# Optimization experiments

Hardware: AMD Instinct MI355X
Metric: run time of the kernel (lower is better)

The kernel has to match this reference:

```python
import jax, jax.numpy as jnp
import numpy as np

B, S, D = 2, 2048, 1024
H = 16
DH = D // H  # 64


def setup_inputs() -> dict:
    key = jax.random.key(0)
    k1, k2, k3 = jax.random.split(key, 3)
    X = jax.random.normal(k1, (B, S, D), dtype=jnp.float32)
    # xavier_normal for Linear(D, 3*D): std = sqrt(2/(fan_in+fan_out))
    std_qkv = float(np.sqrt(2.0 / (D + 3 * D)))
    std_out = float(np.sqrt(2.0 / (D + D)))
    W_qkv = jax.random.normal(k2, (3 * H * DH, D), dtype=jnp.float32) * std_qkv
    W_out = jax.random.normal(k3, (D, H * DH), dtype=jnp.float32) * std_out
    return {"X": X, "W_qkv": W_qkv, "W_out": W_out}


def reference(X, W_qkv, W_out):
    b, s, d = X.shape
    # stacked projection: (b, s, 3*H*DH), then per-head chunk into q,k,v
    qkv = jnp.einsum('bsd,ed->bse', X, W_qkv)
    qkv = qkv.reshape(b, s, H, 3 * DH)
    q, k, v = jnp.split(qkv, 3, axis=-1)  # each (b, s, H, DH)
    scale = 1.0 / jnp.sqrt(jnp.asarray(DH, dtype=X.dtype))
    # naive unfused attention: full [b,H,s,s] score matrix
    scores = jnp.einsum('bqhd,bkhd->bhqk', q, k) * scale
    attn = jax.nn.softmax(scores, axis=-1)
    vals = jnp.einsum('bhqk,bkhd->bqhd', attn, v)
    vals = vals.reshape(b, s, H * DH)
    out = jnp.einsum('bse,de->bsd', vals, W_out)
    return out
```

## Files before the change

### kernel.cpp

```cpp
#include <hip/hip_runtime.h>
#include <cstdint>
#include <cstddef>

typedef __bf16 bf16;
typedef __bf16 bf16x8 __attribute__((ext_vector_type(8)));
typedef __bf16 bf16x2 __attribute__((ext_vector_type(2)));
typedef float  floatx4 __attribute__((ext_vector_type(4)));

typedef __attribute__((address_space(1))) void gvoid_t;
typedef __attribute__((address_space(3))) void lvoid_t;

#define MFMA16(a, b, c) __builtin_amdgcn_mfma_f32_16x16x32_bf16((a), (b), (c), 0, 0, 0)

#if __has_builtin(__builtin_amdgcn_exp2f)
#define EXP2(x) __builtin_amdgcn_exp2f(x)
#else
#define EXP2(x) exp2f(x)
#endif

#define S_TOK 2048
#define E3 3072
#define DMODEL 1024

#define NX 4194304
#define NWQ 3145728
#define NWO 1048576
__global__ __launch_bounds__(256) void cvt_all(const float* __restrict__ X,
                                               const float* __restrict__ Wq,
                                               const float* __restrict__ Wo,
                                               bf16* __restrict__ Xb,
                                               bf16* __restrict__ Wqb,
                                               bf16* __restrict__ Wob) {
  int i = (blockIdx.x * 256 + threadIdx.x) * 8;
  const float* s;
  bf16* d;
  float sc = 1.0f;
  int off;
  if (i < NX) {
    s = X; d = Xb; off = i;
  } else if (i < NX + NWQ) {
    off = i - NX; s = Wq; d = Wqb;
    int row = off >> 10;
    if ((row % 192) < 64) sc = 0.18033688011f;
  } else {
    off = i - NX - NWQ; s = Wo; d = Wob;
  }
  const float4* p = (const float4*)(s + off);
  float4 a = p[0], b = p[1];
  bf16x8 o;
  o[0] = (bf16)(a.x * sc); o[1] = (bf16)(a.y * sc);
  o[2] = (bf16)(a.z * sc); o[3] = (bf16)(a.w * sc);
  o[4] = (bf16)(b.x * sc); o[5] = (bf16)(b.y * sc);
  o[6] = (bf16)(b.z * sc); o[7] = (bf16)(b.w * sc);
  *(bf16x8*)(d + off) = o;
}

__device__ __forceinline__ void gl_lds16(const bf16* g, bf16* l) {
  __builtin_amdgcn_global_load_lds((gvoid_t*)g, (lvoid_t*)l, 16, 0, 0);
}

template <bool OUT_BF16, bool FUSE_V>
__global__ __launch_bounds__(256) void gemm_bt(const bf16* __restrict__ A,
                                               const bf16* __restrict__ Bt,
                                               void* __restrict__ Cv,
                                               bf16* __restrict__ Vt,
                                               int M, int N, int K) {
  __shared__ bf16 sA[128 * 64];
  __shared__ bf16 sB[128 * 64];
  const int tid = threadIdx.x;
  const int wv = tid >> 6, lane = tid & 63;
  const int wr = wv >> 1, wc = wv & 1;
  const int lrow = lane & 15, lgrp = lane >> 4;
  const int R0 = blockIdx.y * 128, C0 = blockIdx.x * 128;

  floatx4 acc[4][4] = {};

  const int srow = lane >> 3;
  const int schk = (lane & 7) ^ srow;
  const bf16* gA = A + (size_t)(R0 + wv * 32 + srow) * K + schk * 8;
  const bf16* gB = Bt + (size_t)(C0 + wv * 32 + srow) * K + schk * 8;
  bf16* lA = sA + wv * 32 * 64;
  bf16* lB = sB + wv * 32 * 64;
  const size_t rs8 = (size_t)8 * K;

  for (int k0 = 0; k0 < K; k0 += 64) {
#pragma unroll
    for (int c = 0; c < 4; c++) {
      gl_lds16(gA + k0 + c * rs8, lA + c * 512);
      gl_lds16(gB + k0 + c * rs8, lB + c * 512);
    }
    __syncthreads();
#pragma unroll
    for (int kk = 0; kk < 2; kk++) {
      bf16x8 af[4], bfr[4];
#pragma unroll
      for (int i = 0; i < 4; i++) {
        int r = wr * 64 + i * 16 + lrow;
        af[i] = *(const bf16x8*)&sA[r * 64 + ((kk * 4 + lgrp) ^ (r & 7)) * 8];
      }
#pragma unroll
      for (int j = 0; j < 4; j++) {
        int r = wc * 64 + j * 16 + lrow;
        bfr[j] = *(const bf16x8*)&sB[r * 64 + ((kk * 4 + lgrp) ^ (r & 7)) * 8];
      }
#pragma unroll
      for (int i = 0; i < 4; i++)
#pragma unroll
        for (int j = 0; j < 4; j++)
          acc[i][j] = MFMA16(af[i], bfr[j], acc[i][j]);
    }
    __syncthreads();
  }

  const int rbase = R0 + wr * 64 + lgrp * 4;
  const int cbase = C0 + wc * 64 + lrow;
  if (OUT_BF16) {
    bf16* C = (bf16*)Cv;
#pragma unroll
    for (int i = 0; i < 4; i++)
#pragma unroll
      for (int j = 0; j < 4; j++) {
        const int col = cbase + j * 16;
        const int m192 = col % 192;
        const int hh = col / 192;
#pragma unroll
        for (int r = 0; r < 4; r++) {
          const int row = rbase + i * 16 + r;
          bf16 val = (bf16)acc[i][j][r];
          bf16* dst;
          if (FUSE_V && m192 >= 128) {
            const int sl = row & 2047;
            const int sp = (sl & ~31) | ((sl & 15) << 1) | ((sl >> 4) & 1);
            dst = Vt + ((size_t)(((row >> 11) * 16 + hh) * 64 + (m192 - 128))) * S_TOK + sp;
          } else {
            dst = C + (size_t)row * N + col;
          }
          *dst = val;
        }
      }
  } else {
    float* C = (float*)Cv;
#pragma unroll
    for (int i = 0; i < 4; i++)
#pragma unroll
      for (int j = 0; j < 4; j++)
#pragma unroll
        for (int r = 0; r < 4; r++)
          C[(size_t)(rbase + i * 16 + r) * N + cbase + j * 16] = acc[i][j][r];
  }
}

__global__ __launch_bounds__(256) void gemm_bt_n64(const bf16* __restrict__ A,
                                                   const bf16* __restrict__ Bt,
                                                   float* __restrict__ C,
                                                   int M, int N, int K) {
  __shared__ bf16 sA[128 * 64];
  __shared__ bf16 sB[64 * 64];
  const int tid = threadIdx.x;
  const int wv = tid >> 6, lane = tid & 63;
  const int wr = wv >> 1, wc = wv & 1;
  const int lrow = lane & 15, lgrp = lane >> 4;
  const int R0 = blockIdx.y * 128, C0 = blockIdx.x * 64;

  floatx4 acc[4][2] = {};

  const int srow = lane >> 3;
  const int schk = (lane & 7) ^ srow;
  const bf16* gA = A + (size_t)(R0 + wv * 32 + srow) * K + schk * 8;
  const bf16* gB = Bt + (size_t)(C0 + wv * 16 + srow) * K + schk * 8;
  bf16* lA = sA + wv * 32 * 64;
  bf16* lB = sB + wv * 16 * 64;
  const size_t rs8 = (size_t)8 * K;

  for (int k0 = 0; k0 < K; k0 += 64) {
#pragma unroll
    for (int c = 0; c < 4; c++) gl_lds16(gA + k0 + c * rs8, lA + c * 512);
#pragma unroll
    for (int c = 0; c < 2; c++) gl_lds16(gB + k0 + c * rs8, lB + c * 512);
    __syncthreads();
#pragma unroll
    for (int kk = 0; kk < 2; kk++) {
      bf16x8 af[4], bfr[2];
#pragma unroll
      for (int i = 0; i < 4; i++) {
        int r = wr * 64 + i * 16 + lrow;
        af[i] = *(const bf16x8*)&sA[r * 64 + ((kk * 4 + lgrp) ^ (r & 7)) * 8];
      }
#pragma unroll
      for (int j = 0; j < 2; j++) {
        int r = wc * 32 + j * 16 + lrow;
        bfr[j] = *(const bf16x8*)&sB[r * 64 + ((kk * 4 + lgrp) ^ (r & 7)) * 8];
      }
#pragma unroll
      for (int i = 0; i < 4; i++)
#pragma unroll
        for (int j = 0; j < 2; j++)
          acc[i][j] = MFMA16(af[i], bfr[j], acc[i][j]);
    }
    __syncthreads();
  }

  const int rbase = R0 + wr * 64 + lgrp * 4;
  const int cbase = C0 + wc * 32 + lrow;
#pragma unroll
  for (int i = 0; i < 4; i++)
#pragma unroll
    for (int j = 0; j < 2; j++)
#pragma unroll
      for (int r = 0; r < 4; r++)
        C[(size_t)(rbase + i * 16 + r) * N + cbase + j * 16] = acc[i][j][r];
}

__global__ __launch_bounds__(512, 2) void attn(const bf16* __restrict__ qkv,
                                               const bf16* __restrict__ Vt,
                                               bf16* __restrict__ vals) {
  __shared__ bf16 sK[2][128 * 64];
  __shared__ bf16 sV[2][64 * 128];
  __shared__ bf16 sP[8][2][640];

  const int tid = threadIdx.x;
  const int wv = tid >> 6, lane = tid & 63;
  const int lrow = lane & 15, lgrp = lane >> 4;
  const int b = blockIdx.z, h = blockIdx.y;
  const int qb = blockIdx.x * 256;

  const int srow = lane >> 3;
  const int scol = (lane & 7) ^ srow;
  const bf16* kg0 = qkv + (size_t)(b * S_TOK + wv * 8 + srow) * E3 + h * 192 + 64 + scol * 8;
  const int vrow = lane >> 4;
  const int vchk = lane & 15;
  const int d0 = wv * 8 + vrow, d1 = d0 + 4;
  const bf16* vg0 = Vt + (size_t)((b * 16 + h) * 64 + d0) * S_TOK + (vchk ^ (d0 & 15)) * 8;
  const bf16* vg1 = Vt + (size_t)((b * 16 + h) * 64 + d1) * S_TOK + (vchk ^ (d1 & 15)) * 8;

  const bf16* qp = qkv + (size_t)(b * S_TOK + qb + wv * 32) * E3 + h * 192;
  bf16x8 qa[2][2];
#pragma unroll
  for (int rt = 0; rt < 2; rt++)
#pragma unroll
    for (int dh = 0; dh < 2; dh++)
      qa[rt][dh] = *(const bf16x8*)(qp + (size_t)(rt * 16 + lrow) * E3 + dh * 32 + lgrp * 8);

  floatx4 O[2][4] = {};
  floatx4 lacc[2] = {};
  bf16x8 ones;
  const bf16 one1 = (bf16)1.0f;
#pragma unroll
  for (int j = 0; j < 8; j++) ones[j] = one1;

  auto stage = [&](int buf, int st) {
    const bf16* kg = kg0 + (size_t)st * 128 * E3;
    gl_lds16(kg, &sK[buf][wv * 512]);
    gl_lds16(kg + (size_t)64 * E3, &sK[buf][4096 + wv * 512]);
    gl_lds16(vg0 + st * 128, &sV[buf][wv * 1024]);
    gl_lds16(vg1 + st * 128, &sV[buf][wv * 1024 + 512]);
  };

  auto compute = [&](int buf) {
#pragma unroll
    for (int g = 0; g < 4; g++) {
      bf16x8 kf[2][2];
#pragma unroll
      for (int t = 0; t < 2; t++)
#pragma unroll
        for (int dh = 0; dh < 2; dh++)
          kf[t][dh] = *(const bf16x8*)&sK[buf][(g * 32 + t * 16 + lrow) * 64 +
                                              ((dh * 4 + lgrp) ^ (lrow & 7)) * 8];
#pragma unroll
      for (int rt = 0; rt < 2; rt++) {
        floatx4 sc0 = {0.f, 0.f, 0.f, 0.f}, sc1 = {0.f, 0.f, 0.f, 0.f};
        sc0 = MFMA16(qa[rt][0], kf[0][0], sc0);
        sc0 = MFMA16(qa[rt][1], kf[0][1], sc0);
        sc1 = MFMA16(qa[rt][0], kf[1][0], sc1);
        sc1 = MFMA16(qa[rt][1], kf[1][1], sc1);
#pragma unroll
        for (int r = 0; r < 4; r++) {
          bf16x2 h2;
          h2[0] = (bf16)EXP2(sc0[r]);
          h2[1] = (bf16)EXP2(sc1[r]);
          *(unsigned*)&sP[wv][rt][(lgrp * 4 + r) * 40 + lrow * 2] =
              __builtin_bit_cast(unsigned, h2);
        }
      }
      bf16x8 vf[4];
#pragma unroll
      for (int dt = 0; dt < 4; dt++)
        vf[dt] = *(const bf16x8*)&sV[buf][(dt * 16 + lrow) * 128 +
                                          ((g * 4 + lgrp) ^ lrow) * 8];
#pragma unroll
      for (int rt = 0; rt < 2; rt++) {
        bf16x8 pf = *(const bf16x8*)&sP[wv][rt][lrow * 40 + lgrp * 8];
#pragma unroll
        for (int dt = 0; dt < 4; dt++) O[rt][dt] = MFMA16(pf, vf[dt], O[rt][dt]);
        lacc[rt] = MFMA16(pf, ones, lacc[rt]);
      }
    }
  };

  stage(0, 0);
  __syncthreads();
#pragma unroll 1
  for (int st = 0; st < 16; st += 2) {
    stage(1, st + 1);
    compute(0);
    __syncthreads();
    if (st + 2 < 16) stage(0, st + 2);
    compute(1);
    __syncthreads();
  }

  bf16* vout = vals + (size_t)(b * S_TOK + qb + wv * 32) * DMODEL + h * 64;
#pragma unroll
  for (int rt = 0; rt < 2; rt++)
#pragma unroll
    for (int r = 0; r < 4; r++) {
      float rinv = __builtin_amdgcn_rcpf(lacc[rt][r]);
#pragma unroll
      for (int dt = 0; dt < 4; dt++)
        vout[(size_t)(rt * 16 + lgrp * 4 + r) * DMODEL + dt * 16 + lrow] =
            (bf16)(O[rt][dt][r] * rinv);
    }
}

extern "C" void kernel_launch(void* const* d_in, const int* in_sizes, int n_in,
                              void* d_out, int out_size, void* d_ws, size_t ws_size,
                              hipStream_t stream) {
  const float* X = (const float*)d_in[0];
  const float* Wqkv = (const float*)d_in[1];
  const float* Wout = (const float*)d_in[2];
  float* out = (float*)d_out;

  char* ws = (char*)d_ws;
  bf16* Xb = (bf16*)(ws);
  bf16* Wqb = (bf16*)(ws + ((size_t)8 << 20));
  bf16* Wob = (bf16*)(ws + ((size_t)14 << 20));
  bf16* qkvb = (bf16*)(ws + ((size_t)16 << 20));
  bf16* Vt = (bf16*)(ws + ((size_t)40 << 20));
  bf16* vals = (bf16*)(ws + ((size_t)48 << 20));

  cvt_all<<<(NX + NWQ + NWO) / 2048, 256, 0, stream>>>(X, Wqkv, Wout, Xb, Wqb, Wob);

  gemm_bt<true, true><<<dim3(24, 32), 256, 0, stream>>>(Xb, Wqb, qkvb, Vt, 4096, 3072, 1024);

  attn<<<dim3(8, 16, 2), 512, 0, stream>>>(qkvb, Vt, vals);

  gemm_bt_n64<<<dim3(16, 32), 256, 0, stream>>>(vals, Wob, out, 4096, 1024, 1024);
}
```

Before: 178.0 us.

## Software-pipeline QK/exp/PV stages in attention with double-buffered P tiles

Splits the per-group attention body into QK, exp-and-write-P, and PV stages, then interleaves them so the exp work of one group overlaps the MFMAs of another. The P scratch tile is double-buffered to allow this. MFMA sections are wrapped in s_setprio raises to favor matrix issue across waves. The grid is also reordered so heads vary fastest, which changes block scheduling and L2 locality; the extra P buffer raises LDS use.

```diff
diff --git a/kernel.cpp b/kernel.cpp
--- a/kernel.cpp
+++ b/kernel.cpp
@@ -216,13 +216,13 @@
                                                bf16* __restrict__ vals) {
   __shared__ bf16 sK[2][128 * 64];
   __shared__ bf16 sV[2][64 * 128];
-  __shared__ bf16 sP[8][2][640];
+  __shared__ bf16 sP[8][2][2][640];
 
   const int tid = threadIdx.x;
   const int wv = tid >> 6, lane = tid & 63;
   const int lrow = lane & 15, lgrp = lane >> 4;
-  const int b = blockIdx.z, h = blockIdx.y;
-  const int qb = blockIdx.x * 256;
+  const int b = blockIdx.z, h = blockIdx.x;
+  const int qb = blockIdx.y * 256;
 
   const int srow = lane >> 3;
   const int scol = (lane & 7) ^ srow;
@@ -243,6 +243,7 @@
 
   floatx4 O[2][4] = {};
   floatx4 lacc[2] = {};
+  floatx4 sc[2][2];
   bf16x8 ones;
   const bf16 one1 = (bf16)1.0f;
 #pragma unroll
@@ -256,45 +257,66 @@
     gl_lds16(vg1 + st * 128, &sV[buf][wv * 1024 + 512]);
   };
 
+  auto qk_g = [&](int buf, int g) {
+    bf16x8 kf[2][2];
+#pragma unroll
+    for (int t = 0; t < 2; t++)
+#pragma unroll
+      for (int dh = 0; dh < 2; dh++)
+        kf[t][dh] = *(const bf16x8*)&sK[buf][(g * 32 + t * 16 + lrow) * 64 +
+                                            ((dh * 4 + lgrp) ^ (lrow & 7)) * 8];
+    __builtin_amdgcn_s_setprio(1);
+#pragma unroll
+    for (int rt = 0; rt < 2; rt++) {
+      floatx4 a0 = {0.f, 0.f, 0.f, 0.f}, a1 = {0.f, 0.f, 0.f, 0.f};
+      a0 = MFMA16(qa[rt][0], kf[0][0], a0);
+      a0 = MFMA16(qa[rt][1], kf[0][1], a0);
+      a1 = MFMA16(qa[rt][0], kf[1][0], a1);
+      a1 = MFMA16(qa[rt][1], kf[1][1], a1);
+      sc[rt][0] = a0;
+      sc[rt][1] = a1;
+    }
+    __builtin_amdgcn_s_setprio(0);
+  };
+
+  auto expw_g = [&](int g) {
+#pragma unroll
+    for (int rt = 0; rt < 2; rt++)
+#pragma unroll
+      for (int r = 0; r < 4; r++) {
+        bf16x2 h2;
+        h2[0] = (bf16)EXP2(sc[rt][0][r]);
+        h2[1] = (bf16)EXP2(sc[rt][1][r]);
+        *(unsigned*)&sP[wv][rt][g & 1][(lgrp * 4 + r) * 40 + lrow * 2] =
+            __builtin_bit_cast(unsigned, h2);
+      }
+  };
+
+  auto pv_g = [&](int buf, int g) {
+    bf16x8 vf[4];
+#pragma unroll
+    for (int dt = 0; dt < 4; dt++)
+      vf[dt] = *(const bf16x8*)&sV[buf][(dt * 16 + lrow) * 128 + ((g * 4 + lgrp) ^ lrow) * 8];
+    __builtin_amdgcn_s_setprio(1);
+#pragma unroll
+    for (int rt = 0; rt < 2; rt++) {
+      bf16x8 pf = *(const bf16x8*)&sP[wv][rt][g & 1][lrow * 40 + lgrp * 8];
+#pragma unroll
+      for (int dt = 0; dt < 4; dt++) O[rt][dt] = MFMA16(pf, vf[dt], O[rt][dt]);
+      lacc[rt] = MFMA16(pf, ones, lacc[rt]);
+    }
+    __builtin_amdgcn_s_setprio(0);
+  };
+
   auto compute = [&](int buf) {
-#pragma unroll
-    for (int g = 0; g < 4; g++) {
-      bf16x8 kf[2][2];
-#pragma unroll
-      for (int t = 0; t < 2; t++)
-#pragma unroll
-        for (int dh = 0; dh < 2; dh++)
-          kf[t][dh] = *(const bf16x8*)&sK[buf][(g * 32 + t * 16 + lrow) * 64 +
-                                              ((dh * 4 + lgrp) ^ (lrow & 7)) * 8];
-#pragma unroll
-      for (int rt = 0; rt < 2; rt++) {
-        floatx4 sc0 = {0.f, 0.f, 0.f, 0.f}, sc1 = {0.f, 0.f, 0.f, 0.f};
-        sc0 = MFMA16(qa[rt][0], kf[0][0], sc0);
-        sc0 = MFMA16(qa[rt][1], kf[0][1], sc0);
-        sc1 = MFMA16(qa[rt][0], kf[1][0], sc1);
-        sc1 = MFMA16(qa[rt][1], kf[1][1], sc1);
-#pragma unroll
-        for (int r = 0; r < 4; r++) {
-          bf16x2 h2;
-          h2[0] = (bf16)EXP2(sc0[r]);
-          h2[1] = (bf16)EXP2(sc1[r]);
-          *(unsigned*)&sP[wv][rt][(lgrp * 4 + r) * 40 + lrow * 2] =
-              __builtin_bit_cast(unsigned, h2);
-        }
-      }
-      bf16x8 vf[4];
-#pragma unroll
-      for (int dt = 0; dt < 4; dt++)
-        vf[dt] = *(const bf16x8*)&sV[buf][(dt * 16 + lrow) * 128 +
-                                          ((g * 4 + lgrp) ^ lrow) * 8];
-#pragma unroll
-      for (int rt = 0; rt < 2; rt++) {
-        bf16x8 pf = *(const bf16x8*)&sP[wv][rt][lrow * 40 + lgrp * 8];
-#pragma unroll
-        for (int dt = 0; dt < 4; dt++) O[rt][dt] = MFMA16(pf, vf[dt], O[rt][dt]);
-        lacc[rt] = MFMA16(pf, ones, lacc[rt]);
-      }
-    }
+    qk_g(buf, 0); expw_g(0);
+    qk_g(buf, 1); expw_g(1);
+    pv_g(buf, 0);
+    qk_g(buf, 2); expw_g(2);
+    pv_g(buf, 1);
+    qk_g(buf, 3); expw_g(3);
+    pv_g(buf, 2);
+    pv_g(buf, 3);
   };
 
   stage(0, 0);
@@ -342,7 +364,7 @@
 
   gemm_bt<true, true><<<dim3(24, 32), 256, 0, stream>>>(Xb, Wqb, qkvb, Vt, 4096, 3072, 1024);
 
-  attn<<<dim3(8, 16, 2), 512, 0, stream>>>(qkvb, Vt, vals);
+  attn<<<dim3(16, 8, 2), 512, 0, stream>>>(qkvb, Vt, vals);
 
   gemm_bt_n64<<<dim3(16, 32), 256, 0, stream>>>(vals, Wob, out, 4096, 1024, 1024);
 }
```

Result: no change. 178.9 us (+0.5%).
